# Kernel optimization log

Measured on AMD Instinct MI355X. Metric: run time of the kernel, lower is better.

Reference implementation:

```python
import jax, jax.numpy as jnp
import numpy as np
import math

N_HEADS = 16
THETA = 10000.0


def setup_inputs() -> dict:
    key = jax.random.key(0)
    ks = jax.random.split(key, 5)
    B, T, D = 4, 2048, 1024
    return {
        "x": jax.random.normal(ks[0], (B, T, D), dtype=jnp.float32),
        "w_qkv": jax.random.normal(ks[1], (3 * D, D), dtype=jnp.float32) * 0.02,
        "b_qkv": jax.random.normal(ks[2], (3 * D,), dtype=jnp.float32) * 0.02,
        "w_out": jax.random.normal(ks[3], (D, D), dtype=jnp.float32) * 0.02,
        "b_out": jax.random.normal(ks[4], (D,), dtype=jnp.float32) * 0.02,
    }


def reference(x, w_qkv, b_qkv, w_out, b_out):
    B, T, D = x.shape
    H = N_HEADS
    hd = D // H
    half = hd // 2

    # fused QKV projection (nn.Linear: y = x @ W^T + b)
    qkv = (x @ w_qkv.T + b_qkv).reshape(B, T, 3, H, hd)
    q, k, v = qkv[:, :, 0], qkv[:, :, 1], qkv[:, :, 2]

    # RoPE: interleaved (even, odd) pairs treated as complex, rotated by e^{i t w}
    inv_freq = 1.0 / (THETA ** (jnp.arange(0, hd, 2, dtype=jnp.float32) / hd))  # [half]
    angles = jnp.arange(T, dtype=jnp.float32)[:, None] * inv_freq[None, :]      # [T, half]
    cos = jnp.cos(angles)[None, :, None, :]  # [1,T,1,half]
    sin = jnp.sin(angles)[None, :, None, :]

    def rotate(t):
        tr = t.reshape(B, T, H, half, 2)
        te, to = tr[..., 0], tr[..., 1]
        rot = jnp.stack([te * cos - to * sin, te * sin + to * cos], axis=-1)
        return rot.reshape(B, T, H, hd).astype(t.dtype)

    q, k = rotate(q), rotate(k)

    # non-causal SDPA, scale = 1/sqrt(head_dim)
    scale = 1.0 / math.sqrt(hd)
    scores = jnp.einsum("bqhd,bkhd->bhqk", q, k) * scale
    attn = jax.nn.softmax(scores, axis=-1)
    out = jnp.einsum("bhqk,bkhd->bqhd", attn, v).reshape(B, T, D)

    return out @ w_out.T + b_out
```

## Files before the change

### kernel.cpp

```cpp
#include <hip/hip_runtime.h>

typedef __attribute__((ext_vector_type(4))) float f32x4;
typedef __attribute__((ext_vector_type(16))) float f32x16;
typedef __attribute__((ext_vector_type(8))) short bf16x8;
typedef __attribute__((ext_vector_type(4))) unsigned u32x4;

__device__ __forceinline__ unsigned short f2bf(float f) {
  unsigned u = __float_as_uint(f);
  u += 0x7fff + ((u >> 16) & 1);
  return (unsigned short)(u >> 16);
}
__device__ __forceinline__ float bf2f(unsigned short h) {
  return __uint_as_float(((unsigned)h) << 16);
}

__device__ __forceinline__ void gload_lds16(const void* g, void* lds) {
  __builtin_amdgcn_global_load_lds(
      (const __attribute__((address_space(1))) unsigned int*)g,
      (__attribute__((address_space(3))) unsigned int*)lds, 16, 0, 0);
}

__global__ void cast3_rope_tbl(const float* __restrict__ x,
                               const float* __restrict__ wq,
                               const float* __restrict__ wo,
                               unsigned short* __restrict__ xb,
                               unsigned short* __restrict__ wqb,
                               unsigned short* __restrict__ wob,
                               float2* __restrict__ cs) {
  if (blockIdx.x >= 12288) {
    int idx = (blockIdx.x - 12288) * blockDim.x + threadIdx.x;
    int t = idx >> 5, i = idx & 31;
    float inv = powf(10000.0f, -(float)(2 * i) / 64.0f);
    float a = (float)t * inv;
    cs[idx] = make_float2(cosf(a), sinf(a));
    return;
  }
  int i = blockIdx.x * blockDim.x + threadIdx.x;
  const float* src;
  unsigned short* dst;
  int off;
  if (i < 2097152) { src = x;  dst = xb;  off = i; }
  else if (i < 2883584) { src = wq; dst = wqb; off = i - 2097152; }
  else { src = wo; dst = wob; off = i - 2883584; }
  float4 v = ((const float4*)src)[off];
  ushort4 o;
  o.x = f2bf(v.x); o.y = f2bf(v.y); o.z = f2bf(v.z); o.w = f2bf(v.w);
  ((ushort4*)dst)[off] = o;
}

__global__ void rope_apply_k(unsigned short* __restrict__ qkv,
                             const float2* __restrict__ cs) {
  int idx = blockIdx.x * blockDim.x + threadIdx.x;
  int i4 = idx & 7;
  int h = (idx >> 3) & 15;
  int t = (idx >> 7) & 2047;
  int b = idx >> 18;
  unsigned short* p =
      qkv + ((size_t)((b << 11) + t)) * 3072 + 1024 + h * 64 + i4 * 8;
  bf16x8 v = *(const bf16x8*)p;
  const float2* c4 = cs + (t << 5) + i4 * 4;
#pragma unroll
  for (int j = 0; j < 4; ++j) {
    const float2 cn = c4[j];
    const float e = bf2f((unsigned short)v[2 * j]);
    const float o = bf2f((unsigned short)v[2 * j + 1]);
    v[2 * j]     = (short)f2bf(e * cn.x - o * cn.y);
    v[2 * j + 1] = (short)f2bf(e * cn.y + o * cn.x);
  }
  *(bf16x8*)p = v;
}

template <int OUT_BF16>
__global__ __launch_bounds__(512, 2) void gemm_bt_p(
    const unsigned short* __restrict__ A, const unsigned short* __restrict__ B,
    const float* __restrict__ bias, void* __restrict__ Cout,
    int M, int N, int K) {
  __shared__ unsigned short lA[3 * 8192];
  __shared__ unsigned short lB[3 * 4096];

  const int tiles_n = N >> 7;
  const int swz = (blockIdx.x & 7) * (gridDim.x >> 3) + (blockIdx.x >> 3);
  const int bm = swz / tiles_n;
  const int bn = swz % tiles_n;
  const int m0 = bm << 8, n0 = bn << 7;
  const int tid = threadIdx.x;
  const int w = tid >> 6, l = tid & 63;
  const int l15 = l & 15, lq = l >> 4;
  const int wm = w >> 2, wn = w & 3;

  const int sl8 = l >> 3, sc = l & 7;

  f32x4 acc[8][2] = {};

#define STAGE_HALF(J, RS)                                                     \
  if ((J) < 32) {                                                             \
    const int k0_ = (J) * 32;                                                 \
    _Pragma("unroll")                                                         \
    for (int i_ = 0; i_ < 2; ++i_) {                                          \
      const int line = i_ * 64 + w * 8 + sl8;                                 \
      const int lc = sc ^ (line & 7);                                         \
      const int row = 2 * line + (lc >> 2);                                   \
      gload_lds16(A + (size_t)(m0 + row) * K + k0_ + (lc & 3) * 8,            \
                  &lA[(RS) * 8192 + line * 64 + sc * 8]);                     \
    }                                                                         \
    {                                                                         \
      const int line = w * 8 + sl8;                                           \
      const int lc = sc ^ (line & 7);                                         \
      const int row = 2 * line + (lc >> 2);                                   \
      gload_lds16(B + (size_t)(n0 + row) * K + k0_ + (lc & 3) * 8,            \
                  &lB[(RS) * 4096 + line * 64 + sc * 8]);                     \
    }                                                                         \
  }

  STAGE_HALF(0, 0);
  STAGE_HALF(1, 1);

  int rb = 0;
  for (int j = 0; j < 32; ++j) {
    if (j < 31)
      asm volatile("s_waitcnt vmcnt(3)" ::: "memory");
    else
      asm volatile("s_waitcnt vmcnt(0)" ::: "memory");
    __builtin_amdgcn_s_barrier();

    bf16x8 af[8], bfr[2];
#pragma unroll
    for (int mi = 0; mi < 8; ++mi) {
      const int row = wm * 128 + mi * 16 + l15;
      const int line = row >> 1;
      const int pc = (((row & 1) * 4 + lq) ^ (line & 7));
      af[mi] = *(const bf16x8*)&lA[rb * 8192 + line * 64 + pc * 8];
    }
#pragma unroll
    for (int ni = 0; ni < 2; ++ni) {
      const int row = wn * 32 + ni * 16 + l15;
      const int line = row >> 1;
      const int pc = (((row & 1) * 4 + lq) ^ (line & 7));
      bfr[ni] = *(const bf16x8*)&lB[rb * 4096 + line * 64 + pc * 8];
    }

    const int rs = rb == 0 ? 2 : rb - 1;
    STAGE_HALF(j + 2, rs);

    __builtin_amdgcn_s_setprio(1);
#pragma unroll
    for (int mi = 0; mi < 8; ++mi)
#pragma unroll
      for (int ni = 0; ni < 2; ++ni)
        acc[mi][ni] = __builtin_amdgcn_mfma_f32_16x16x32_bf16(
            af[mi], bfr[ni], acc[mi][ni], 0, 0, 0);
    __builtin_amdgcn_s_setprio(0);

    rb = rb == 2 ? 0 : rb + 1;
  }
#undef STAGE_HALF

#pragma unroll
  for (int ni = 0; ni < 2; ++ni) {
    const int c = n0 + wn * 32 + ni * 16 + l15;
    const float bv = bias[c];
#pragma unroll
    for (int mi = 0; mi < 8; ++mi) {
#pragma unroll
      for (int jj = 0; jj < 4; ++jj) {
        const int r = m0 + wm * 128 + mi * 16 + lq * 4 + jj;
        const float v = acc[mi][ni][jj] + bv;
        if (OUT_BF16)
          ((unsigned short*)Cout)[(size_t)r * N + c] = f2bf(v);
        else
          ((float*)Cout)[(size_t)r * N + c] = v;
      }
    }
  }
}

#define PACKPV(SCV, KS)                                                        \
  do {                                                                         \
    unsigned xa, xb, ya, yb;                                                   \
    asm("v_cvt_pk_bf16_f32 %0, %1, %2"                                         \
        : "=v"(xa) : "v"(SCV[((KS) & 1) * 8 + 0]), "v"(SCV[((KS) & 1) * 8 + 1])); \
    asm("v_cvt_pk_bf16_f32 %0, %1, %2"                                         \
        : "=v"(xb) : "v"(SCV[((KS) & 1) * 8 + 2]), "v"(SCV[((KS) & 1) * 8 + 3])); \
    asm("v_cvt_pk_bf16_f32 %0, %1, %2"                                         \
        : "=v"(ya) : "v"(SCV[((KS) & 1) * 8 + 4]), "v"(SCV[((KS) & 1) * 8 + 5])); \
    asm("v_cvt_pk_bf16_f32 %0, %1, %2"                                         \
        : "=v"(yb) : "v"(SCV[((KS) & 1) * 8 + 6]), "v"(SCV[((KS) & 1) * 8 + 7])); \
    asm("v_permlane32_swap_b32 %0, %1" : "+v"(xa), "+v"(ya));                  \
    asm("v_permlane32_swap_b32 %0, %1" : "+v"(xb), "+v"(yb));                  \
    u32x4 pw;                                                                  \
    pw[0] = xa; pw[1] = xb; pw[2] = ya; pw[3] = yb;                            \
    const bf16x8 pa = __builtin_bit_cast(bf16x8, pw);                          \
    {                                                                          \
      const bf16x8 vf = *(const bf16x8*)                                       \
          &lVc[l31 * 72 + ((16 * (KS) + 8 * hi) ^ (l31 & 0x38))];              \
      o0 = __builtin_amdgcn_mfma_f32_32x32x16_bf16(pa, vf, o0, 0, 0, 0);       \
    }                                                                          \
    {                                                                          \
      const int vrow = 32 + l31;                                               \
      const bf16x8 vf = *(const bf16x8*)                                       \
          &lVc[vrow * 72 + ((16 * (KS) + 8 * hi) ^ (vrow & 0x38))];            \
      o1 = __builtin_amdgcn_mfma_f32_32x32x16_bf16(pa, vf, o1, 0, 0, 0);       \
    }                                                                          \
  } while (0)

#define EXP_HALF(SV)                                                           \
  do {                                                                         \
    _Pragma("unroll")                                                          \
    for (int r = 0; r < 16; r += 2) {                                          \
      float a0 = __builtin_fmaf(SV[r], L2E, -m2);                              \
      float a1 = __builtin_fmaf(SV[r + 1], L2E, -m2);                          \
      float p0, p1;                                                            \
      asm("v_exp_f32 %0, %1" : "=v"(p0) : "v"(a0));                            \
      asm("v_exp_f32 %0, %1" : "=v"(p1) : "v"(a1));                            \
      SV[r] = p0;                                                              \
      SV[r + 1] = p1;                                                          \
      rsa += p0;                                                               \
      rsb += p1;                                                               \
    }                                                                          \
  } while (0)

__global__ __launch_bounds__(512, 4) void attn_fwd(
    const unsigned short* __restrict__ qkv, unsigned short* __restrict__ aout,
    const float2* __restrict__ cs) {
  __shared__ unsigned short lK[2 * 64 * 64];
  __shared__ unsigned short lVt[2 * 64 * 72];

  const int g = blockIdx.x;
  const int xcd = g & 7;
  const int j2 = g >> 3;
  const int bh = ((j2 >> 3) << 3) + xcd;
  const int qt = j2 & 7;
  const int h = bh & 15, b = bh >> 4;

  const int tid = threadIdx.x;
  const int w = tid >> 6, l = tid & 63;
  const int l31 = l & 31, hi = l >> 5;
  const int l7 = l & 7;

  const size_t bt_base = (size_t)(b * 2048) * 3072;
  const int qbase = qt * 256 + w * 32;

  const unsigned short* Qp =
      qkv + bt_base + (size_t)(qbase + l31) * 3072 + h * 64 + hi * 8;
  const float2* csrow = cs + (size_t)(qbase + l31) * 32;
  bf16x8 qf[4];
#pragma unroll
  for (int s = 0; s < 4; ++s) {
    bf16x8 q = *(const bf16x8*)(Qp + 16 * s);
#pragma unroll
    for (int j = 0; j < 4; ++j) {
      const float2 cn = csrow[8 * s + 4 * hi + j];
      const float e = bf2f((unsigned short)q[2 * j]);
      const float o = bf2f((unsigned short)q[2 * j + 1]);
      q[2 * j]     = (short)f2bf((e * cn.x - o * cn.y) * 0.125f);
      q[2 * j + 1] = (short)f2bf((e * cn.y + o * cn.x) * 0.125f);
    }
    qf[s] = q;
  }

  const unsigned short* Kp = qkv + bt_base + 1024 + h * 64;
  const unsigned short* Vp = qkv + bt_base + 2048 + h * 64;

  const int krow = l >> 3;
  const int kcol = ((l & 7) ^ (l >> 3)) << 3;

  const int vr = tid >> 3;
  const int vc0 = (tid & 7) << 3;
  const int vx = vc0;

  f32x16 o0 = {}, o1 = {};
  float m_run = -1e30f, lsum = 0.f;
  bf16x8 v0;
  const float L2E = 1.4426950408889634f;

  {
    gload_lds16(Kp + (size_t)(w * 8 + krow) * 3072 + kcol, &lK[(w * 8) * 64]);
    const unsigned short* vb = Vp + (size_t)vr * 3072 + vc0;
    v0 = *(const bf16x8*)vb;
  }
  __syncthreads();
#pragma unroll
  for (int i2 = 0; i2 < 8; ++i2)
    lVt[(vc0 + i2) * 72 + (vr ^ vx)] = (unsigned short)v0[i2];
  __syncthreads();

  for (int t = 0; t < 32; ++t) {
    const int cur = t & 1;
    const unsigned short* lKc = lK + cur * 4096;
    const unsigned short* lVc = lVt + cur * 4608;
    const bool stage = (t < 31);

    if (stage) {
      const unsigned short* kb = Kp + (size_t)(t + 1) * 64 * 3072;
      gload_lds16(kb + (size_t)(w * 8 + krow) * 3072 + kcol,
                  lK + (cur ^ 1) * 4096 + (w * 8) * 64);
    }

    f32x16 s0 = {}, s1 = {};
    __builtin_amdgcn_s_setprio(1);
#pragma unroll
    for (int s = 0; s < 4; ++s) {
      bf16x8 kf = *(const bf16x8*)&lKc[l31 * 64 + (((2 * s + hi) ^ l7) << 3)];
      s0 = __builtin_amdgcn_mfma_f32_32x32x16_bf16(kf, qf[s], s0, 0, 0, 0);
    }
#pragma unroll
    for (int s = 0; s < 4; ++s) {
      bf16x8 kf = *(const bf16x8*)&lKc[(32 + l31) * 64 + (((2 * s + hi) ^ l7) << 3)];
      s1 = __builtin_amdgcn_mfma_f32_32x32x16_bf16(kf, qf[s], s1, 0, 0, 0);
    }
    __builtin_amdgcn_s_setprio(0);

    if (stage) {
      const unsigned short* vb =
          Vp + (size_t)(t + 1) * 64 * 3072 + (size_t)vr * 3072 + vc0;
      v0 = *(const bf16x8*)vb;
    }

    float rsa = 0.f, rsb = 0.f;
    float m2;
    {
      float pmax = -1e30f;
#pragma unroll
      for (int r = 0; r < 16; r += 2) {
        float t0, t1;
        asm("v_max3_f32 %0, %1, %2, %3"
            : "=v"(t0) : "v"(s0[r]), "v"(s0[r + 1]), "v"(pmax));
        asm("v_max3_f32 %0, %1, %2, %3"
            : "=v"(t1) : "v"(s1[r]), "v"(s1[r + 1]), "v"(t0));
        pmax = t1;
      }
      pmax = fmaxf(pmax, __shfl_xor(pmax, 32));
      if (!__all(pmax <= m_run + 8.0f)) {
        const float mn = fmaxf(m_run, pmax);
        const float alpha = __expf(m_run - mn);
        m_run = mn;
        lsum *= alpha;
#pragma unroll
        for (int r = 0; r < 16; ++r) {
          const float ar = __shfl(alpha, (r & 3) + 8 * (r >> 2) + 4 * hi);
          o0[r] *= ar;
          o1[r] *= ar;
        }
      }
      m2 = m_run * L2E;
    }

    EXP_HALF(s0);

    if (stage) {
      unsigned short* lVn = lVt + (cur ^ 1) * 4608;
#pragma unroll
      for (int i2 = 0; i2 < 8; ++i2)
        lVn[(vc0 + i2) * 72 + (vr ^ vx)] = (unsigned short)v0[i2];
    }

    __builtin_amdgcn_s_setprio(1);
    PACKPV(s0, 0);
    PACKPV(s0, 1);
    __builtin_amdgcn_s_setprio(0);

    EXP_HALF(s1);

    __builtin_amdgcn_s_setprio(1);
    PACKPV(s1, 2);
    PACKPV(s1, 3);
    __builtin_amdgcn_s_setprio(0);

    float rs = rsa + rsb;
    rs += __shfl_xor(rs, 32);
    lsum += rs;

    __syncthreads();
  }

  const float linv = 1.0f / lsum;
#pragma unroll
  for (int r = 0; r < 16; ++r) {
    const int crow = (r & 3) + 8 * (r >> 2) + 4 * hi;
    const float lr = __shfl(linv, crow);
    unsigned short* orow =
        aout + (size_t)(b * 2048 + qbase + crow) * 1024 + h * 64 + l31;
    orow[0] = f2bf(o0[r] * lr);
    orow[32] = f2bf(o1[r] * lr);
  }
}

extern "C" void kernel_launch(void* const* d_in, const int* in_sizes, int n_in,
                              void* d_out, int out_size, void* d_ws, size_t ws_size,
                              hipStream_t stream) {
  const float* x     = (const float*)d_in[0];
  const float* w_qkv = (const float*)d_in[1];
  const float* b_qkv = (const float*)d_in[2];
  const float* w_out = (const float*)d_in[3];
  const float* b_out = (const float*)d_in[4];
  float* out = (float*)d_out;

  char* ws = (char*)d_ws;
  unsigned short* x_bf    = (unsigned short*)(ws);
  unsigned short* wqkv_bf = (unsigned short*)(ws + 16777216);
  unsigned short* wout_bf = (unsigned short*)(ws + 23068672);
  unsigned short* qkv     = (unsigned short*)(ws + 25165824);
  unsigned short* aout    = (unsigned short*)(ws + 75497472);
  float2* cs              = (float2*)(ws + 92274688);

  cast3_rope_tbl<<<12544, 256, 0, stream>>>(x, w_qkv, w_out,
                                            x_bf, wqkv_bf, wout_bf, cs);

  gemm_bt_p<1><<<768, 512, 0, stream>>>(x_bf, wqkv_bf, b_qkv, qkv,
                                        8192, 3072, 1024);
  rope_apply_k<<<1048576 / 256, 256, 0, stream>>>(qkv, cs);
  attn_fwd<<<512, 512, 0, stream>>>(qkv, aout, cs);
  gemm_bt_p<0><<<256, 512, 0, stream>>>(aout, wout_bf, b_out, out,
                                        8192, 1024, 1024);
}
```

Before: 204.0 us.

## Process attention key tile as two 32-row subtiles with per-subtile online softmax

Each 64-key tile is now handled as two sequential 32-key subtiles. Each subtile does its own QK MFMAs, max reduction, optional rescale, exp and PV accumulation, and only one S accumulator is live at a time. This lowers register pressure so the kernel can sustain 4 waves per SIMD, and it lets one subtile's softmax interleave with another's matrix work. In exchange it doubles the max/rescale checks and cross-lane shuffles per tile, and it moves the V global load after the first subtile.

```diff
diff --git a/kernel.cpp b/kernel.cpp
--- a/kernel.cpp
+++ b/kernel.cpp
@@ -203,20 +203,57 @@
     }                                                                          \
   } while (0)
 
-#define EXP_HALF(SV)                                                           \
+#define SUBTILE(KR, KS0)                                                       \
   do {                                                                         \
+    f32x16 s = {};                                                             \
+    __builtin_amdgcn_s_setprio(1);                                             \
+    _Pragma("unroll")                                                          \
+    for (int ss = 0; ss < 4; ++ss) {                                           \
+      bf16x8 kf = *(const bf16x8*)                                             \
+          &lKc[((KR) + l31) * 64 + (((2 * ss + hi) ^ l7) << 3)];               \
+      s = __builtin_amdgcn_mfma_f32_32x32x16_bf16(kf, qf[ss], s, 0, 0, 0);     \
+    }                                                                          \
+    __builtin_amdgcn_s_setprio(0);                                             \
+    float pmax = -1e30f;                                                       \
     _Pragma("unroll")                                                          \
     for (int r = 0; r < 16; r += 2) {                                          \
-      float a0 = __builtin_fmaf(SV[r], L2E, -m2);                              \
-      float a1 = __builtin_fmaf(SV[r + 1], L2E, -m2);                          \
+      float t0;                                                                \
+      asm("v_max3_f32 %0, %1, %2, %3"                                          \
+          : "=v"(t0) : "v"(s[r]), "v"(s[r + 1]), "v"(pmax));                   \
+      pmax = t0;                                                               \
+    }                                                                          \
+    pmax = fmaxf(pmax, __shfl_xor(pmax, 32));                                  \
+    if (!__all(pmax <= m_run + 8.0f)) {                                        \
+      const float mn = fmaxf(m_run, pmax);                                     \
+      const float alpha = __expf(m_run - mn);                                  \
+      m_run = mn;                                                              \
+      lsum *= alpha;                                                           \
+      _Pragma("unroll")                                                        \
+      for (int r = 0; r < 16; ++r) {                                           \
+        const float ar = __shfl(alpha, (r & 3) + 8 * (r >> 2) + 4 * hi);       \
+        o0[r] *= ar;                                                           \
+        o1[r] *= ar;                                                           \
+      }                                                                        \
+    }                                                                          \
+    const float m2 = m_run * L2E;                                              \
+    float rsa = 0.f, rsb = 0.f;                                                \
+    _Pragma("unroll")                                                          \
+    for (int r = 0; r < 16; r += 2) {                                          \
+      float a0 = __builtin_fmaf(s[r], L2E, -m2);                               \
+      float a1 = __builtin_fmaf(s[r + 1], L2E, -m2);                           \
       float p0, p1;                                                            \
       asm("v_exp_f32 %0, %1" : "=v"(p0) : "v"(a0));                            \
       asm("v_exp_f32 %0, %1" : "=v"(p1) : "v"(a1));                            \
-      SV[r] = p0;                                                              \
-      SV[r + 1] = p1;                                                          \
-      rsa += p0;                                                               \
-      rsb += p1;                                                               \
-    }                                                                          \
+      s[r] = p0; s[r + 1] = p1;                                                \
+      rsa += p0; rsb += p1;                                                    \
+    }                                                                          \
+    float rsl = rsa + rsb;                                                     \
+    rsl += __shfl_xor(rsl, 32);                                                \
+    lsum += rsl;                                                               \
+    __builtin_amdgcn_s_setprio(1);                                             \
+    PACKPV(s, (KS0));                                                          \
+    PACKPV(s, (KS0) + 1);                                                      \
+    __builtin_amdgcn_s_setprio(0);                                             \
   } while (0)
 
 __global__ __launch_bounds__(512, 4) void attn_fwd(
@@ -296,19 +333,7 @@
                   lK + (cur ^ 1) * 4096 + (w * 8) * 64);
     }
 
-    f32x16 s0 = {}, s1 = {};
-    __builtin_amdgcn_s_setprio(1);
-#pragma unroll
-    for (int s = 0; s < 4; ++s) {
-      bf16x8 kf = *(const bf16x8*)&lKc[l31 * 64 + (((2 * s + hi) ^ l7) << 3)];
-      s0 = __builtin_amdgcn_mfma_f32_32x32x16_bf16(kf, qf[s], s0, 0, 0, 0);
-    }
-#pragma unroll
-    for (int s = 0; s < 4; ++s) {
-      bf16x8 kf = *(const bf16x8*)&lKc[(32 + l31) * 64 + (((2 * s + hi) ^ l7) << 3)];
-      s1 = __builtin_amdgcn_mfma_f32_32x32x16_bf16(kf, qf[s], s1, 0, 0, 0);
-    }
-    __builtin_amdgcn_s_setprio(0);
+    SUBTILE(0, 0);
 
     if (stage) {
       const unsigned short* vb =
@@ -316,36 +341,7 @@
       v0 = *(const bf16x8*)vb;
     }
 
-    float rsa = 0.f, rsb = 0.f;
-    float m2;
-    {
-      float pmax = -1e30f;
-#pragma unroll
-      for (int r = 0; r < 16; r += 2) {
-        float t0, t1;
-        asm("v_max3_f32 %0, %1, %2, %3"
-            : "=v"(t0) : "v"(s0[r]), "v"(s0[r + 1]), "v"(pmax));
-        asm("v_max3_f32 %0, %1, %2, %3"
-            : "=v"(t1) : "v"(s1[r]), "v"(s1[r + 1]), "v"(t0));
-        pmax = t1;
-      }
-      pmax = fmaxf(pmax, __shfl_xor(pmax, 32));
-      if (!__all(pmax <= m_run + 8.0f)) {
-        const float mn = fmaxf(m_run, pmax);
-        const float alpha = __expf(m_run - mn);
-        m_run = mn;
-        lsum *= alpha;
-#pragma unroll
-        for (int r = 0; r < 16; ++r) {
-          const float ar = __shfl(alpha, (r & 3) + 8 * (r >> 2) + 4 * hi);
-          o0[r] *= ar;
-          o1[r] *= ar;
-        }
-      }
-      m2 = m_run * L2E;
-    }
-
-    EXP_HALF(s0);
+    SUBTILE(32, 2);
 
     if (stage) {
       unsigned short* lVn = lVt + (cur ^ 1) * 4608;
@@ -353,23 +349,6 @@
       for (int i2 = 0; i2 < 8; ++i2)
         lVn[(vc0 + i2) * 72 + (vr ^ vx)] = (unsigned short)v0[i2];
     }
-
-    __builtin_amdgcn_s_setprio(1);
-    PACKPV(s0, 0);
-    PACKPV(s0, 1);
-    __builtin_amdgcn_s_setprio(0);
-
-    EXP_HALF(s1);
-
-    __builtin_amdgcn_s_setprio(1);
-    PACKPV(s1, 2);
-    PACKPV(s1, 3);
-    __builtin_amdgcn_s_setprio(0);
-
-    float rs = rsa + rsb;
-    rs += __shfl_xor(rs, 32);
-    lsum += rs;
-
     __syncthreads();
   }
 
```

After: 201.7 us. About the same (-1.1%).
